# Optimization experiments

Measured on AMD Instinct MI355X. Metric: run time of the kernel, lower is better.

## Reference

```python
import jax, jax.numpy as jnp
import numpy as np

NUM_CHANNELS = 64
NUM_FILTERS = 2
B, H, W = 4, 256, 256
K_SLOTS = NUM_FILTERS * 9 + 1  # 19 (9 taps per filter + skip slot)


def setup_inputs() -> dict:
    key = jax.random.key(0)
    k1, k2, k3 = jax.random.split(key, 3)
    k = jax.random.normal(k1, (B, K_SLOTS, H, W), dtype=jnp.float32)
    x = jax.random.normal(k2, (B, NUM_FILTERS * NUM_CHANNELS, H, W), dtype=jnp.float32)
    skip = jax.random.normal(k3, (B, NUM_CHANNELS, H, W), dtype=jnp.float32)
    return {"k": k, "x": x, "skip": skip}


def _patches3x3(x):
    # x: [B, C, H, W] -> [B, C, 9, H, W]; matches F.unfold(kernel=3, pad=1)
    # reshaped to (B, C, 9, H, W): tap order is row-major (ki, kj).
    Bx, Cx, Hx, Wx = x.shape
    xp = jnp.pad(x, ((0, 0), (0, 0), (1, 1), (1, 1)))
    taps = [xp[:, :, i:i + Hx, j:j + Wx] for i in range(3) for j in range(3)]
    return jnp.stack(taps, axis=2)


def reference(k, x, skip):
    # per-filter 3x3 patches, concatenated along the tap/slot axis
    plist = [_patches3x3(x[:, f * NUM_CHANNELS:(f + 1) * NUM_CHANNELS])
             for f in range(NUM_FILTERS)]
    plist.append(skip[:, :, None])                 # skip slot: [B, C, 1, H, W]
    patches = jnp.concatenate(plist, axis=2)       # [B, C, 19, H, W]
    # per-pixel predicted kernel broadcast over channels, reduce over slots
    return jnp.sum(patches * k[:, None], axis=2)   # [B, C, H, W]
```

## Files before the change

### kernel.cpp

```cpp
#include <hip/hip_runtime.h>


constexpr int Hh = 256;
constexpr int Ww = 256;
constexpr int HW = Hh * Ww;
constexpr int C  = 64;
constexpr int NF = 2;
constexpr int KS = 19;

__global__ __launch_bounds__(256) void filt_kernel(
    const float* __restrict__ kk,
    const float* __restrict__ x,
    const float* __restrict__ skip,
    float* __restrict__ out) {
  const int blk  = blockIdx.x;
  const int cg   = blk & 3;
  const int h    = (blk >> 2) & 255;
  const int b    = blk >> 10;
  const int tid  = threadIdx.x;
  const int lane = tid & 63;
  const int wv   = tid >> 6;
  const int w0   = lane << 2;

  __shared__ float lds_k[KS][Ww];

  const float* kb = kk + (size_t)b * KS * HW + (size_t)h * Ww;
  for (int s = wv; s < KS; s += 4)
    *(float4*)&lds_k[s][w0] = *(const float4*)(kb + (size_t)s * HW + w0);
  __syncthreads();

  const int c0 = cg * 16 + wv * 4;
  const float* xb = x    + (size_t)b * NF * C * HW;
  const float* sb = skip + ((size_t)b * C + c0) * HW + (size_t)h * Ww + w0;
  float*       ob = out  + ((size_t)b * C + c0) * HW + (size_t)h * Ww + w0;

  float4 k18 = *(const float4*)&lds_k[18][w0];
  float acc[4][4];
#pragma unroll
  for (int ch = 0; ch < 4; ++ch) {
    float4 sv = *(const float4*)(sb + (size_t)ch * HW);
    acc[ch][0] = k18.x * sv.x; acc[ch][1] = k18.y * sv.y;
    acc[ch][2] = k18.z * sv.z; acc[ch][3] = k18.w * sv.w;
  }

#pragma unroll
  for (int f = 0; f < NF; ++f) {
    const float* xf = xb + (size_t)(f * C + c0) * HW;
#pragma unroll
    for (int ki = 0; ki < 3; ++ki) {
      const int hh = h + ki - 1;
      if (hh < 0 || hh >= Hh) continue;
      const float* xr = xf + (size_t)hh * Ww + w0;

      float v[4][6];
#pragma unroll
      for (int ch = 0; ch < 4; ++ch) {
        float4 xm = *(const float4*)(xr + (size_t)ch * HW);
        v[ch][1] = xm.x; v[ch][2] = xm.y; v[ch][3] = xm.z; v[ch][4] = xm.w;
      }
#pragma unroll
      for (int ch = 0; ch < 4; ++ch) {
        float lf = __shfl_up(v[ch][4], 1);
        float rg = __shfl_down(v[ch][1], 1);
        v[ch][0] = (lane == 0)  ? 0.0f : lf;
        v[ch][5] = (lane == 63) ? 0.0f : rg;
      }
#pragma unroll
      for (int kj = 0; kj < 3; ++kj) {
        const int s = f * 9 + ki * 3 + kj;
        float4 kw = *(const float4*)&lds_k[s][w0];
#pragma unroll
        for (int ch = 0; ch < 4; ++ch) {
          acc[ch][0] = fmaf(kw.x, v[ch][0 + kj], acc[ch][0]);
          acc[ch][1] = fmaf(kw.y, v[ch][1 + kj], acc[ch][1]);
          acc[ch][2] = fmaf(kw.z, v[ch][2 + kj], acc[ch][2]);
          acc[ch][3] = fmaf(kw.w, v[ch][3 + kj], acc[ch][3]);
        }
      }
    }
  }

#pragma unroll
  for (int ch = 0; ch < 4; ++ch) {
    float4 o = make_float4(acc[ch][0], acc[ch][1], acc[ch][2], acc[ch][3]);
    *(float4*)(ob + (size_t)ch * HW) = o;
  }
}

extern "C" void kernel_launch(void* const* d_in, const int* in_sizes, int n_in,
                              void* d_out, int out_size, void* d_ws, size_t ws_size,
                              hipStream_t stream) {
  const float* kk = (const float*)d_in[0];
  const float* x  = (const float*)d_in[1];
  const float* sk = (const float*)d_in[2];
  float* out = (float*)d_out;

  dim3 grid(4 * Hh * 4);
  dim3 block(256);
  filt_kernel<<<grid, block, 0, stream>>>(kk, x, sk, out);
}
```

Measured before the change: 278.9 us.

## Issue all x/skip loads before LDS staging and halve channels per block

Moves every global load of x rows and skip for the thread's channels ahead of the k-slot LDS fill and barrier, so that memory latency overlaps the staging of k. Each wave now handles 2 channels instead of 4 and the grid is doubled. A launch-bounds occupancy hint is also added. The cost is that k slots are re-read from global and LDS twice as often, since each block covers fewer channels per row.

```diff
diff --git a/kernel.cpp b/kernel.cpp
--- a/kernel.cpp
+++ b/kernel.cpp
@@ -8,15 +8,15 @@
 constexpr int NF = 2;
 constexpr int KS = 19;
 
-__global__ __launch_bounds__(256) void filt_kernel(
+__global__ __launch_bounds__(256, 4) void filt_kernel(
     const float* __restrict__ kk,
     const float* __restrict__ x,
     const float* __restrict__ skip,
     float* __restrict__ out) {
   const int blk  = blockIdx.x;
-  const int cg   = blk & 3;
-  const int h    = (blk >> 2) & 255;
-  const int b    = blk >> 10;
+  const int cg   = blk & 7;
+  const int h    = (blk >> 3) & 255;
+  const int b    = blk >> 11;
   const int tid  = threadIdx.x;
   const int lane = tid & 63;
   const int wv   = tid >> 6;
@@ -24,42 +24,55 @@
 
   __shared__ float lds_k[KS][Ww];
 
+  const int c0 = cg * 8 + wv * 2;
+
+  const float* xb = x    + (size_t)b * NF * C * HW;
+  const float* sb = skip + ((size_t)b * C + c0) * HW + (size_t)h * Ww + w0;
+
+  float4 sv[2];
+  float4 xv[2][6];
+#pragma unroll
+  for (int ch = 0; ch < 2; ++ch) {
+    sv[ch] = *(const float4*)(sb + (size_t)ch * HW);
+#pragma unroll
+    for (int f = 0; f < NF; ++f) {
+#pragma unroll
+      for (int ki = 0; ki < 3; ++ki) {
+        const int hh = h + ki - 1;
+        if (hh >= 0 && hh < Hh) {
+          const float* xr = xb + (size_t)(f * C + c0 + ch) * HW
+                               + (size_t)hh * Ww + w0;
+          xv[ch][f * 3 + ki] = *(const float4*)xr;
+        } else {
+          xv[ch][f * 3 + ki] = make_float4(0.f, 0.f, 0.f, 0.f);
+        }
+      }
+    }
+  }
+
   const float* kb = kk + (size_t)b * KS * HW + (size_t)h * Ww;
   for (int s = wv; s < KS; s += 4)
     *(float4*)&lds_k[s][w0] = *(const float4*)(kb + (size_t)s * HW + w0);
   __syncthreads();
 
-  const int c0 = cg * 16 + wv * 4;
-  const float* xb = x    + (size_t)b * NF * C * HW;
-  const float* sb = skip + ((size_t)b * C + c0) * HW + (size_t)h * Ww + w0;
-  float*       ob = out  + ((size_t)b * C + c0) * HW + (size_t)h * Ww + w0;
-
   float4 k18 = *(const float4*)&lds_k[18][w0];
-  float acc[4][4];
+  float acc[2][4];
 #pragma unroll
-  for (int ch = 0; ch < 4; ++ch) {
-    float4 sv = *(const float4*)(sb + (size_t)ch * HW);
-    acc[ch][0] = k18.x * sv.x; acc[ch][1] = k18.y * sv.y;
-    acc[ch][2] = k18.z * sv.z; acc[ch][3] = k18.w * sv.w;
+  for (int ch = 0; ch < 2; ++ch) {
+    acc[ch][0] = k18.x * sv[ch].x; acc[ch][1] = k18.y * sv[ch].y;
+    acc[ch][2] = k18.z * sv[ch].z; acc[ch][3] = k18.w * sv[ch].w;
   }
 
 #pragma unroll
   for (int f = 0; f < NF; ++f) {
-    const float* xf = xb + (size_t)(f * C + c0) * HW;
 #pragma unroll
     for (int ki = 0; ki < 3; ++ki) {
-      const int hh = h + ki - 1;
-      if (hh < 0 || hh >= Hh) continue;
-      const float* xr = xf + (size_t)hh * Ww + w0;
-
-      float v[4][6];
+      const int r = f * 3 + ki;
+      float v[2][6];
 #pragma unroll
-      for (int ch = 0; ch < 4; ++ch) {
-        float4 xm = *(const float4*)(xr + (size_t)ch * HW);
-        v[ch][1] = xm.x; v[ch][2] = xm.y; v[ch][3] = xm.z; v[ch][4] = xm.w;
-      }
-#pragma unroll
-      for (int ch = 0; ch < 4; ++ch) {
+      for (int ch = 0; ch < 2; ++ch) {
+        v[ch][1] = xv[ch][r].x; v[ch][2] = xv[ch][r].y;
+        v[ch][3] = xv[ch][r].z; v[ch][4] = xv[ch][r].w;
         float lf = __shfl_up(v[ch][4], 1);
         float rg = __shfl_down(v[ch][1], 1);
         v[ch][0] = (lane == 0)  ? 0.0f : lf;
@@ -70,7 +83,7 @@
         const int s = f * 9 + ki * 3 + kj;
         float4 kw = *(const float4*)&lds_k[s][w0];
 #pragma unroll
-        for (int ch = 0; ch < 4; ++ch) {
+        for (int ch = 0; ch < 2; ++ch) {
           acc[ch][0] = fmaf(kw.x, v[ch][0 + kj], acc[ch][0]);
           acc[ch][1] = fmaf(kw.y, v[ch][1 + kj], acc[ch][1]);
           acc[ch][2] = fmaf(kw.z, v[ch][2 + kj], acc[ch][2]);
@@ -80,8 +93,9 @@
     }
   }
 
+  float* ob = out + ((size_t)b * C + c0) * HW + (size_t)h * Ww + w0;
 #pragma unroll
-  for (int ch = 0; ch < 4; ++ch) {
+  for (int ch = 0; ch < 2; ++ch) {
     float4 o = make_float4(acc[ch][0], acc[ch][1], acc[ch][2], acc[ch][3]);
     *(float4*)(ob + (size_t)ch * HW) = o;
   }
@@ -95,7 +109,7 @@
   const float* sk = (const float*)d_in[2];
   float* out = (float*)d_out;
 
-  dim3 grid(4 * Hh * 4);
+  dim3 grid(4 * Hh * 8);
   dim3 block(256);
   filt_kernel<<<grid, block, 0, stream>>>(kk, x, sk, out);
 }
```

Result: slower. 293.3 us (+5.2%).
